# Optimization experiments

Hardware: AMD Instinct MI355X
Metric: run time of the kernel (lower is better)

The kernel has to match this reference:

```python
import math
import jax, jax.numpy as jnp
import numpy as np
from jax import lax

B, S, D = 2, 1024, 768
H, E, DH = 12, 8, 64          # n_head, num_experts, head dim
KA = 1                        # top-k experts per head (attention)
KF = 2                        # top-k experts per token (FFN)
DFF = 2048
EMA_DECAY = 0.99
CAP_FACTOR = 1.25
NEG_INF = -1e9


def setup_inputs() -> dict:
    key = jax.random.key(0)
    ks = jax.random.split(key, 16)
    sc = 0.02
    x = jax.random.normal(ks[0], (B, S, D), jnp.float32)
    causal = jnp.tril(jnp.ones((S, S), jnp.float32))
    mask = jnp.where(causal > 0, 0.0, NEG_INF).astype(jnp.float32)
    return {
        "x": x,
        "mask": mask,
        "W_q": jax.random.normal(ks[1], (D, D), jnp.float32) * sc,
        "W_k": jax.random.normal(ks[2], (D, D), jnp.float32) * sc,
        "W_v": jax.random.normal(ks[3], (H, E, DH, DH), jnp.float32) * sc,
        "W_o": jax.random.normal(ks[4], (H, E, DH, DH), jnp.float32) * sc,
        "W_router": jax.random.normal(ks[5], (D, H * E), jnp.float32) * sc,
        "g1": jnp.ones((D,), jnp.float32),
        "b1": jnp.zeros((D,), jnp.float32),
        "g2": jnp.ones((D,), jnp.float32),
        "b2": jnp.zeros((D,), jnp.float32),
        "gate_ff": jax.random.normal(ks[6], (D, E), jnp.float32) * sc,
        "W1": jax.random.normal(ks[7], (E, D, DFF), jnp.float32) * sc,
        "W2": jax.random.normal(ks[8], (E, DFF, D), jnp.float32) * sc,
    }


def layer_norm(x, g, b, eps=1e-5):
    m = jnp.mean(x, -1, keepdims=True)
    v = jnp.var(x, -1, keepdims=True)
    return (x - m) * lax.rsqrt(v + eps) * g + b


def head_switch_attention(x, mask, W_q, W_k, W_v, W_o, W_router):
    b, s, d = x.shape
    q = (x @ W_q).reshape(b, s, H, DH)
    k = (x @ W_k).reshape(b, s, H, DH)
    scores = jnp.einsum("bshd,bthd->bhst", q, k) / math.sqrt(DH) + mask
    p_attn = jax.nn.softmax(scores, axis=-1)          # (B,H,S,S)
    gate_logits = (x @ W_router).reshape(b, s, H, E)
    topk_scores, topk_idx = lax.top_k(gate_logits, KA)  # (B,S,H,KA)
    probs = jax.nn.softmax(topk_scores, axis=-1)
    x_h = x.reshape(b, s, H, DH)
    # value projections for all experts (small d_h x d_h GEMMs)
    v_all = jnp.einsum("bshd,hedf->bshef", x_h, W_v)
    y = jnp.zeros_like(x_h)
    hard_counts = jnp.zeros((H, E), jnp.float32)
    for slot in range(KA):
        oh = jax.nn.one_hot(topk_idx[..., slot], E, dtype=x.dtype)  # (B,S,H,E)
        v_sel = jnp.einsum("bshef,bshe->bshf", v_all, oh)
        # faithful to original einsum 'bhst,hbsd->hbtd' (sums over s)
        attn_out = jnp.einsum("bhst,bshf->bthf", p_attn, v_sel)
        o_all = jnp.einsum("bthf,hefg->btheg", attn_out, W_o)
        o_sel = jnp.einsum("btheg,bthe->bthg", o_all, oh)
        y = y + o_sel * probs[..., slot][..., None]
        hard_counts = hard_counts + lax.stop_gradient(oh).sum((0, 1))
    y = y.reshape(b, s, d)
    # EMA buffers start at zero -> ema = (1-decay)*hard/denom
    ema = hard_counts / (b * s * KA) * (1.0 - EMA_DECAY)
    p_lb = ema / (ema.sum() + 1e-9)
    aux = (p_lb * p_lb).sum() * E * H
    return y, aux


def moe_ffn(x, gate_ff, W1, W2):
    b, s, d = x.shape
    gate_logits = x @ gate_ff                      # (B,S,E), eval: no noise
    topk_scores, topk_idx = lax.top_k(gate_logits, KF)
    probs = jax.nn.softmax(topk_scores, axis=-1)   # (B,S,KF)
    capacity = math.ceil(CAP_FACTOR * (b * s) / E)
    flat_idx = topk_idx.reshape(-1)                # (B*S*KF,)
    oh_flat = jax.nn.one_hot(flat_idx, E, dtype=jnp.float32)
    tokens_so_far = jnp.cumsum(oh_flat, axis=0)
    keep = jnp.take_along_axis(tokens_so_far <= capacity, flat_idx[:, None], axis=1)[:, 0]
    probs = probs * keep.reshape(b, s, KF).astype(probs.dtype)
    probs = probs / (probs.sum(-1, keepdims=True) + 1e-9)
    oh = jax.nn.one_hot(topk_idx, E, dtype=probs.dtype)   # (B,S,KF,E)
    w = (probs[..., None] * oh).sum(2).reshape(b * s, E)  # combined weight per (token, expert)
    xf = x.reshape(b * s, d)
    yf = jnp.zeros_like(xf)
    for e in range(E):
        # scaling applied BEFORE ReLU, matching original x_sel = x * weight
        xe = xf * w[:, e:e + 1]
        yf = yf + jnp.maximum(xe @ W1[e], 0.0) @ W2[e]
    token_ctr = ((probs > 0)[..., None].astype(jnp.float32) * oh).sum((0, 1, 2))
    imp_ctr = (probs[..., None] * oh).sum((0, 1, 2))
    aux = ((token_ctr / token_ctr.sum()) * (imp_ctr / imp_ctr.sum())).sum() * E
    return yf.reshape(b, s, d), aux


def reference(x, mask, W_q, W_k, W_v, W_o, W_router, g1, b1, g2, b2, gate_ff, W1, W2):
    # pre-norm transformer block: x + Attn(LN(x)); x + MoEFFN(LN(x))
    a, aux1 = head_switch_attention(layer_norm(x, g1, b1), mask, W_q, W_k, W_v, W_o, W_router)
    x1 = x + a  # dropout is identity in eval
    f, aux2 = moe_ffn(layer_norm(x1, g2, b2), gate_ff, W1, W2)
    return x1 + f, aux1 + aux2
```

## Files before the change

### kernel.cpp

```cpp
#include <hip/hip_runtime.h>
#include <hip/hip_bf16.h>
#include <cstdint>

typedef __hip_bfloat16 bf16;
typedef __attribute__((ext_vector_type(8))) __bf16 bfrag;
typedef __attribute__((ext_vector_type(4))) float f32x4;

#define B_    2
#define S_    1024
#define D_    768
#define H_    12
#define E_    8
#define DH_   64
#define DFF_  2048
#define CAP_  320
#define CAPP_ 384
#define NTOK  (B_*S_)
#define NTH   (NTOK*H_)
#define QKLD  1536
#define NHE   (H_*E_)

__device__ __forceinline__ void stage16(const bf16* g, bf16* ldsLane){
#if __has_builtin(__builtin_amdgcn_global_load_lds)
  __builtin_amdgcn_global_load_lds((const __attribute__((address_space(1))) unsigned int*)g,
                                   (__attribute__((address_space(3))) unsigned int*)ldsLane, 16, 0, 0);
#else
  *(bfrag*)ldsLane = *(const bfrag*)g;
#endif
}

__device__ __forceinline__ void transp_tile_bf16(const float* __restrict__ src, bf16* __restrict__ dst,
                                                 int N, int K, int n0, int k0, int tid, float (*t)[64])
{
  int chunk = tid & 15, rgrp = tid >> 4;
#pragma unroll
  for (int rr=0; rr<8; rr++){
    int row = rr*16 + rgrp;
    float4 v = *(const float4*)(src + (long)(k0+row)*N + n0 + chunk*4);
    *(float4*)&t[row][((chunk ^ (row>>3)) & 15)*4] = v;
  }
  __syncthreads();
#pragma unroll
  for (int it=0; it<4; it++){
    int slot = it*256 + tid;
    int n = slot >> 4, kc = slot & 15;
    union { bfrag f; bf16 h[8]; } o;
#pragma unroll
    for (int i=0;i<8;i++){
      int row = kc*8 + i;
      o.h[i] = __float2bfloat16(t[row][n ^ (kc*4)]);
    }
    *(bfrag*)(dst + (long)(n0+n)*K + k0 + kc*8) = o.f;
  }
}

__global__ __launch_bounds__(256)
void transp_qkr(const float* __restrict__ Wq, const float* __restrict__ Wk,
                const float* __restrict__ Wr, bf16* __restrict__ WcatB, float* __restrict__ WrT)
{
  __shared__ float t[128][64];
  int bid = blockIdx.x, tid = threadIdx.x;
  if (bid < 144){
    const float* src; bf16* dst; int r;
    if (bid < 72){ src = Wq; dst = WcatB; r = bid; }
    else         { src = Wk; dst = WcatB + (long)768*768; r = bid - 72; }
    transp_tile_bf16(src, dst, 768, 768, (r%12)*64, (r/12)*128, tid, t);
  } else {
    int r = bid - 144;
    int n0 = (r % 3)*32, k0 = (r / 3)*64;
    int chunk = tid & 7, row2 = tid >> 3;
#pragma unroll
    for (int rr=0; rr<2; rr++){
      int row = rr*32 + row2;
      float4 v = *(const float4*)(Wr + (long)(k0+row)*96 + n0 + chunk*4);
      *(float4*)&t[row][chunk*4] = v;
    }
    __syncthreads();
    int chunkw = tid & 15, ng = tid >> 4;
#pragma unroll
    for (int rr=0; rr<2; rr++){
      int n = rr*16 + ng;
      float4 o;
      o.x = t[chunkw*4+0][n]; o.y = t[chunkw*4+1][n];
      o.z = t[chunkw*4+2][n]; o.w = t[chunkw*4+3][n];
      *(float4*)(WrT + (long)(n0+n)*768 + k0 + chunkw*4) = o;
    }
  }
}

__global__ __launch_bounds__(256)
void gemm_bn64(const bf16* __restrict__ A, const bf16* __restrict__ Bt,
               void* __restrict__ C, void* __restrict__ C2,
               int M, int N, int K, long sA, long sB, long sC, int relu, int outBf, int kSplit)
{
  int nwg = gridDim.x*gridDim.y*gridDim.z;
  int bid = blockIdx.x + gridDim.x*(blockIdx.y + gridDim.y*blockIdx.z);
  int nid = (bid & 7)*(nwg >> 3) + (bid >> 3);
  int bx = nid % gridDim.x;
  int t1 = nid / gridDim.x;
  int by = t1 % gridDim.y;
  int bz = t1 / gridDim.y;
  int e  = bz / kSplit, kc = bz - e*kSplit;
  A  += (long)e*sA;
  Bt += (long)e*sB;
  int kLen = K / kSplit, kBase = kc*kLen;
  int m0 = by*128, n0 = bx*64;
  __shared__ bf16 As[2][128*32];
  __shared__ bf16 Bs[2][64*32];
  int tid = threadIdx.x;
  int w = tid >> 6, lane = tid & 63;
  int quad = lane >> 4, l16 = lane & 15;
  int wm = w*32;
  f32x4 acc[2][4] = {};
  int srow = (lane >> 2);
  int gsw  = ((lane & 3) ^ (srow & 3))*8;
  const bf16* aBase = A + (long)m0*K;
  const bf16* bBase = Bt + (long)n0*K;
  int xr = (l16 & 3);
  int nIt = kLen >> 5;
  {
    int k0 = kBase;
#pragma unroll
    for (int j=0;j<2;j++){
      int c = w*2 + j, row = c*16 + srow;
      stage16(aBase + (long)row*K + k0 + gsw, As[0] + c*512 + lane*8);
    }
    int rowb = w*16 + srow;
    stage16(bBase + (long)rowb*K + k0 + gsw, Bs[0] + w*512 + lane*8);
  }
  int cur = 0;
  for (int it=0; it<nIt; ++it){
    __syncthreads();
    if (it+1 < nIt){
      int k0 = kBase + (it+1)*32;
      int nb = cur^1;
#pragma unroll
      for (int j=0;j<2;j++){
        int c = w*2 + j, row = c*16 + srow;
        stage16(aBase + (long)row*K + k0 + gsw, As[nb] + c*512 + lane*8);
      }
      int rowb = w*16 + srow;
      stage16(bBase + (long)rowb*K + k0 + gsw, Bs[nb] + w*512 + lane*8);
    }
    const bf16* Ac = As[cur];
    const bf16* Bc = Bs[cur];
    bfrag af[2], bfv[4];
#pragma unroll
    for (int t=0;t<2;t++) af[t]  = *(const bfrag*)(Ac + (wm + t*16 + l16)*32 + ((quad ^ xr)*8));
#pragma unroll
    for (int t=0;t<4;t++) bfv[t] = *(const bfrag*)(Bc + (t*16 + l16)*32 + ((quad ^ xr)*8));
#pragma unroll
    for (int ti=0;ti<2;ti++)
#pragma unroll
      for (int tj=0;tj<4;tj++)
        acc[ti][tj] = __builtin_amdgcn_mfma_f32_16x16x32_bf16(af[ti], bfv[tj], acc[ti][tj], 0, 0, 0);
    cur ^= 1;
  }
  long zoff = (long)e*sC;
  void* Cp = kc ? C2 : C;
  if (outBf){
    bf16* Cb = (bf16*)Cp + zoff;
#pragma unroll
    for (int ti=0;ti<2;ti++)
#pragma unroll
      for (int tj=0;tj<4;tj++)
#pragma unroll
        for (int r=0;r<4;r++){
          int row = m0 + wm + ti*16 + quad*4 + r;
          int col = n0 + tj*16 + l16;
          float v = acc[ti][tj][r];
          if (relu) v = fmaxf(v, 0.f);
          Cb[(long)row*N + col] = __float2bfloat16(v);
        }
  } else {
    float* Cf = (float*)Cp + zoff;
#pragma unroll
    for (int ti=0;ti<2;ti++)
#pragma unroll
      for (int tj=0;tj<4;tj++)
#pragma unroll
        for (int r=0;r<4;r++){
          int row = m0 + wm + ti*16 + quad*4 + r;
          int col = n0 + tj*16 + l16;
          float v = acc[ti][tj][r];
          if (relu) v = fmaxf(v, 0.f);
          Cf[(long)row*N + col] = v;
        }
  }
}

__global__ __launch_bounds__(256)
void gemm_ffn1(const float* __restrict__ ln2, const bf16* __restrict__ Bt, bf16* __restrict__ C,
               const int* __restrict__ lTok, const float* __restrict__ lW, const int* __restrict__ gCnt)
{
  int nwg = gridDim.x*gridDim.y*gridDim.z;
  int bid = blockIdx.x + gridDim.x*(blockIdx.y + gridDim.y*blockIdx.z);
  int nid = (bid & 7)*(nwg >> 3) + (bid >> 3);
  int bx = nid % gridDim.x;
  int t1 = nid / gridDim.x;
  int by = t1 % gridDim.y;
  int e  = t1 / gridDim.y;
  int m0 = by*128;
  const bf16* bBase = Bt + (long)e*2048*768 + (long)(bx*64)*768;
  __shared__ bf16 As[2][128*32];
  __shared__ bf16 Bs[2][64*32];
  int tid = threadIdx.x;
  int w = tid >> 6, lane = tid & 63;
  int quad = lane >> 4, l16 = lane & 15;
  int wm = w*32;
  f32x4 acc[2][4] = {};
  int srow = (lane >> 2);
  int gsw  = ((lane & 3) ^ (srow & 3))*8;
  int xr = (l16 & 3);
  int cnt = gCnt[e];
  int tokA[2]; float wA[2];
#pragma unroll
  for (int j=0;j<2;j++){
    int row = m0 + (w*2+j)*16 + srow;
    bool live = row < cnt;
    tokA[j] = live ? lTok[e*CAP_ + row] : 0;
    wA[j]   = live ? lW[e*CAP_ + row]   : 0.f;
  }
  const int nIt = 24;
  {
#pragma unroll
    for (int j=0;j<2;j++){
      const float* src = ln2 + (long)tokA[j]*D_ + gsw;
      float4 a0 = *(const float4*)(src);
      float4 a1 = *(const float4*)(src+4);
      union { bfrag f; bf16 h[8]; } o;
      o.h[0]=__float2bfloat16(a0.x*wA[j]); o.h[1]=__float2bfloat16(a0.y*wA[j]);
      o.h[2]=__float2bfloat16(a0.z*wA[j]); o.h[3]=__float2bfloat16(a0.w*wA[j]);
      o.h[4]=__float2bfloat16(a1.x*wA[j]); o.h[5]=__float2bfloat16(a1.y*wA[j]);
      o.h[6]=__float2bfloat16(a1.z*wA[j]); o.h[7]=__float2bfloat16(a1.w*wA[j]);
      *(bfrag*)(As[0] + (w*2+j)*512 + lane*8) = o.f;
    }
    int rowb = w*16 + srow;
    stage16(bBase + (long)rowb*768 + gsw, Bs[0] + w*512 + lane*8);
  }
  int cur = 0;
  for (int it=0; it<nIt; ++it){
    __syncthreads();
    float4 a0[2], a1[2];
    if (it+1 < nIt){
      int k0 = (it+1)*32;
#pragma unroll
      for (int j=0;j<2;j++){
        const float* src = ln2 + (long)tokA[j]*D_ + k0 + gsw;
        a0[j] = *(const float4*)(src);
        a1[j] = *(const float4*)(src+4);
      }
      int rowb = w*16 + srow;
      stage16(bBase + (long)rowb*768 + k0 + gsw, Bs[cur^1] + w*512 + lane*8);
    }
    const bf16* Ac = As[cur];
    const bf16* Bc = Bs[cur];
    bfrag af[2], bfv[4];
#pragma unroll
    for (int t=0;t<2;t++) af[t]  = *(const bfrag*)(Ac + (wm + t*16 + l16)*32 + ((quad ^ xr)*8));
#pragma unroll
    for (int t=0;t<4;t++) bfv[t] = *(const bfrag*)(Bc + (t*16 + l16)*32 + ((quad ^ xr)*8));
#pragma unroll
    for (int ti=0;ti<2;ti++)
#pragma unroll
      for (int tj=0;tj<4;tj++)
        acc[ti][tj] = __builtin_amdgcn_mfma_f32_16x16x32_bf16(af[ti], bfv[tj], acc[ti][tj], 0, 0, 0);
    if (it+1 < nIt){
      int nb = cur^1;
#pragma unroll
      for (int j=0;j<2;j++){
        union { bfrag f; bf16 h[8]; } o;
        o.h[0]=__float2bfloat16(a0[j].x*wA[j]); o.h[1]=__float2bfloat16(a0[j].y*wA[j]);
        o.h[2]=__float2bfloat16(a0[j].z*wA[j]); o.h[3]=__float2bfloat16(a0[j].w*wA[j]);
        o.h[4]=__float2bfloat16(a1[j].x*wA[j]); o.h[5]=__float2bfloat16(a1[j].y*wA[j]);
        o.h[6]=__float2bfloat16(a1[j].z*wA[j]); o.h[7]=__float2bfloat16(a1[j].w*wA[j]);
        *(bfrag*)(As[nb] + (w*2+j)*512 + lane*8) = o.f;
      }
    }
    cur ^= 1;
  }
  bf16* Cb = C + (long)e*CAPP_*DFF_;
#pragma unroll
  for (int ti=0;ti<2;ti++)
#pragma unroll
    for (int tj=0;tj<4;tj++)
#pragma unroll
      for (int r=0;r<4;r++){
        int row = m0 + wm + ti*16 + quad*4 + r;
        int col = bx*64 + tj*16 + l16;
        Cb[(long)row*DFF_ + col] = __float2bfloat16(fmaxf(acc[ti][tj][r], 0.f));
      }
}

__global__ __launch_bounds__(256)
void ln_kernel(const float* __restrict__ src, const float* __restrict__ g, const float* __restrict__ bb,
               float* __restrict__ dstF, bf16* __restrict__ dstB,
               const float* __restrict__ gateW, float* __restrict__ glog2)
{
  int row = blockIdx.x, tid = threadIdx.x;
  __shared__ float red[256];
  __shared__ float gsum[4][E_];
  float v[3];
#pragma unroll
  for (int j=0;j<3;j++) v[j] = src[(long)row*D_ + tid + j*256];
  float s = v[0]+v[1]+v[2];
  red[tid]=s; __syncthreads();
  for (int o=128;o>0;o>>=1){ if(tid<o) red[tid]+=red[tid+o]; __syncthreads(); }
  float mean = red[0]*(1.0f/D_);
  __syncthreads();
  float sq = 0.f;
#pragma unroll
  for (int j=0;j<3;j++){ float d=v[j]-mean; sq += d*d; }
  red[tid]=sq; __syncthreads();
  for (int o=128;o>0;o>>=1){ if(tid<o) red[tid]+=red[tid+o]; __syncthreads(); }
  float rstd = rsqrtf(red[0]*(1.0f/D_) + 1e-5f);
  float ov[3];
#pragma unroll
  for (int j=0;j<3;j++){
    int d = tid + j*256;
    float o = (v[j]-mean)*rstd*g[d] + bb[d];
    ov[j] = o;
    dstF[(long)row*D_+d] = o;
    if (dstB) dstB[(long)row*D_+d] = __float2bfloat16(o);
  }
  if (gateW){
    float gp[E_] = {};
#pragma unroll
    for (int j=0;j<3;j++){
      int d = tid + j*256;
      const float* gw = gateW + (long)d*E_;
#pragma unroll
      for (int e=0;e<E_;e++) gp[e] += ov[j]*gw[e];
    }
#pragma unroll
    for (int off=1; off<64; off<<=1)
#pragma unroll
      for (int e=0;e<E_;e++) gp[e] += __shfl_xor(gp[e], off);
    if ((tid & 63) == 0)
#pragma unroll
      for (int e=0;e<E_;e++) gsum[tid>>6][e] = gp[e];
    __syncthreads();
    if (tid < E_)
      glog2[(long)row*E_ + tid] = gsum[0][tid]+gsum[1][tid]+gsum[2][tid]+gsum[3][tid];
  }
}

#define RTOK 4
__global__ __launch_bounds__(768)
void router_argmax(const float* __restrict__ ln1, const float* __restrict__ WrT,
                   int* __restrict__ eidx, int* __restrict__ gHist,
                   int* __restrict__ hCnt, int* __restrict__ hList)
{
  int tok0 = blockIdx.x*RTOK;
  int tid = threadIdx.x;
  int col = tid >> 3, seg = tid & 7;
  __shared__ float xrow[RTOK][D_];
  __shared__ float logits[RTOK][96];
  for (int i=tid; i<RTOK*D_; i+=768){
    int t = i / D_, dpos = i - t*D_;
    xrow[t][dpos] = ln1[(long)(tok0+t)*D_ + dpos];
  }
  __syncthreads();
  const float* wrow = WrT + (long)col*D_;
  float acc[RTOK] = {};
#pragma unroll
  for (int j=0;j<24;j++){
    int dbase = j*32 + seg*4;
    float4 w = *(const float4*)(wrow + dbase);
#pragma unroll
    for (int t=0;t<RTOK;t++){
      float4 xv = *(const float4*)(&xrow[t][dbase]);
      acc[t] += xv.x*w.x + xv.y*w.y + xv.z*w.z + xv.w*w.w;
    }
  }
#pragma unroll
  for (int off=1; off<8; off<<=1)
#pragma unroll
    for (int t=0;t<RTOK;t++) acc[t] += __shfl_xor(acc[t], off);
  if (seg == 0)
#pragma unroll
    for (int t=0;t<RTOK;t++) logits[t][col] = acc[t];
  __syncthreads();
  if (tid < RTOK*H_){
    int t = tid / H_, h = tid % H_;
    const float* p = &logits[t][h*8];
    float best = p[0]; int bi = 0;
#pragma unroll
    for (int e=1;e<8;e++){ float v=p[e]; if (v > best){ best=v; bi=e; } }
    int tok = tok0 + t;
    eidx[tok*H_ + h] = bi;
    atomicAdd(&gHist[h*E_ + bi], 1);
    int he = h*E_ + bi;
    int pos = atomicAdd(&hCnt[he], 1);
    hList[he*NTOK + pos] = tok;
  }
}

__global__ __launch_bounds__(256)
void vsel_b(const float* __restrict__ ln1, const float* __restrict__ Wv,
            const int* __restrict__ hCnt, const int* __restrict__ hList,
            bf16* __restrict__ vT)
{
  int he = blockIdx.x;
  int h = he >> 3;
  __shared__ float Ws[DH_*DH_];
  __shared__ float xsh[4][DH_];
  int tid = threadIdx.x;
  const float* W = Wv + (long)he*DH_*DH_;
  for (int i=tid; i<DH_*DH_; i+=256) Ws[i] = W[i];
  int cnt = hCnt[he];
  __syncthreads();
  int w = tid >> 6, lane = tid & 63;
  const int* lst = hList + (long)he*NTOK;
  for (int i = blockIdx.y*4 + w; i < cnt; i += 32){
    int tok = lst[i];
    int b = tok >> 10, s = tok & 1023;
    xsh[w][lane] = ln1[(long)tok*D_ + h*DH_ + lane];
    float acc = 0.f;
#pragma unroll 8
    for (int d=0; d<DH_; d++) acc += xsh[w][d]*Ws[d*DH_ + lane];
    vT[((long)(b*H_+h)*DH_ + lane)*S_ + s] = __float2bfloat16(acc);
  }
}

__global__ __launch_bounds__(256)
void attn_stats_mfma(const bf16* __restrict__ qkB, float* __restrict__ gM, float* __restrict__ gL,
                     const float* __restrict__ W1, const float* __restrict__ W2,
                     bf16* __restrict__ WT1, bf16* __restrict__ WT2)
{
  __shared__ __align__(16) char smem[32768];
  int tid = threadIdx.x;
  if (blockIdx.z >= 2){
    int flat = (blockIdx.z - 2)*96 + blockIdx.y*8 + blockIdx.x;
    const float* src; int N, K, bx, by; bf16* dst;
    if (flat < 1536){ int e = flat/192, r = flat - e*192;
      src = W1 + (long)e*768*2048; N = 2048; K = 768;  bx = r % 32; by = r / 32;
      dst = WT1 + (long)e*2048*768;
    } else { int f2 = flat - 1536; int e = f2/192, r = f2 - e*192;
      src = W2 + (long)e*2048*768; N = 768;  K = 2048; bx = r % 12; by = r / 12;
      dst = WT2 + (long)e*768*2048;
    }
    transp_tile_bf16(src, dst, N, K, bx*64, by*128, tid, (float(*)[64])smem);
    return;
  }
  bf16* ldsQ = (bf16*)smem;
  int h = blockIdx.y, b = blockIdx.z;
  int w = tid >> 6, lane = tid & 63;
  int quad = lane >> 4, l16 = lane & 15;
  int x7 = l16 & 7;
  const bf16* kbase = qkB + ((long)(b*S_))*QKLD + 768 + h*DH_;
  for (int half=0; half<2; half++){
    int s0 = (half ? (S_/64 - 1 - blockIdx.x) : blockIdx.x)*64;
    __syncthreads();
    const bf16* qbase = qkB + ((long)(b*S_ + s0))*QKLD + h*DH_;
#pragma unroll
    for (int j=0;j<2;j++){
      int c = j*256 + tid;
      int row = c >> 3;
      int gs = ((c & 7) ^ (row & 7))*8;
      stage16(qbase + (long)row*QKLD + gs, ldsQ + c*8);
      stage16(kbase + (long)row*QKLD + gs, (bf16*)(smem + 8192) + c*8);
    }
    float m_ln[4] = {-1e30f,-1e30f,-1e30f,-1e30f};
    float l_ln[4] = {0.f,0.f,0.f,0.f};
    int ttEnd = s0 >> 6;
    int cur = 0;
    for (int tt=0; tt<=ttEnd; tt++){
      __syncthreads();
      if (tt < ttEnd){
        bf16* Kn = (bf16*)(smem + 8192 + ((cur^1) << 13));
#pragma unroll
        for (int j=0;j<2;j++){
          int c = j*256 + tid;
          int row = c >> 3;
          int gs = ((c & 7) ^ (row & 7))*8;
          stage16(kbase + (long)((tt+1)*64 + row)*QKLD + gs, Kn + c*8);
        }
      }
      const bf16* Kc = (const bf16*)(smem + 8192 + (cur << 13));
      bfrag af0 = *(const bfrag*)(ldsQ + (w*16 + l16)*64 + ((quad     ^ x7)*8));
      bfrag af1 = *(const bfrag*)(ldsQ + (w*16 + l16)*64 + (((quad+4) ^ x7)*8));
      f32x4 cfr[4];
#pragma unroll
      for (int j=0;j<4;j++){
        bfrag b0 = *(const bfrag*)(Kc + (j*16 + l16)*64 + ((quad     ^ x7)*8));
        bfrag b1 = *(const bfrag*)(Kc + (j*16 + l16)*64 + (((quad+4) ^ x7)*8));
        f32x4 z = {};
        z = __builtin_amdgcn_mfma_f32_16x16x32_bf16(af0, b0, z, 0,0,0);
        z = __builtin_amdgcn_mfma_f32_16x16x32_bf16(af1, b1, z, 0,0,0);
        cfr[j] = z;
      }
#pragma unroll
      for (int r=0;r<4;r++){
        int s_g = s0 + w*16 + quad*4 + r;
        float v0 = (tt*64      + l16 <= s_g) ? cfr[0][r]*0.125f : -1e30f;
        float v1 = (tt*64 + 16 + l16 <= s_g) ? cfr[1][r]*0.125f : -1e30f;
        float v2 = (tt*64 + 32 + l16 <= s_g) ? cfr[2][r]*0.125f : -1e30f;
        float v3 = (tt*64 + 48 + l16 <= s_g) ? cfr[3][r]*0.125f : -1e30f;
        float mt = fmaxf(fmaxf(v0,v1), fmaxf(v2,v3));
        float mn = fmaxf(m_ln[r], mt);
        l_ln[r] = l_ln[r]*__expf(m_ln[r]-mn)
                + ((__expf(v0-mn)+__expf(v1-mn)) + (__expf(v2-mn)+__expf(v3-mn)));
        m_ln[r] = mn;
      }
      cur ^= 1;
    }
#pragma unroll
    for (int r=0;r<4;r++){
      float mf = m_ln[r];
#pragma unroll
      for (int mm=1; mm<16; mm<<=1) mf = fmaxf(mf, __shfl_xor(mf, mm));
      float lf = l_ln[r]*__expf(m_ln[r]-mf);
#pragma unroll
      for (int mm=1; mm<16; mm<<=1) lf += __shfl_xor(lf, mm);
      if (l16 == 0){
        long basei = ((long)(b*H_ + h))*S_ + s0 + w*16 + quad*4 + r;
        gM[basei] = mf; gL[basei] = lf;
      }
    }
  }
}

__global__ __launch_bounds__(256)
void attn_pv(const bf16* __restrict__ qkB, const bf16* __restrict__ vT,
             const float* __restrict__ gM, const float* __restrict__ gL, float* __restrict__ aoH)
{
  int h = blockIdx.y, b = blockIdx.z;
  int bh = b*H_ + h;
  int tid = threadIdx.x;
  int w = tid >> 6, lane = tid & 63;
  int quad = lane >> 4, l16 = lane & 15;
  int x7 = l16 & 7;
  __shared__ bf16 ldsK[64*64];
  __shared__ bf16 ldsQ[2][64*64];
  __shared__ bf16 ldsV[2][64*64];
  __shared__ bf16 ldsS[64*72];
  __shared__ float smx[2][64], sli[2][64];
  const bf16* qbase = qkB + ((long)(b*S_))*QKLD + h*DH_;
  const bf16* vbase = vT + ((long)bh*DH_)*S_;
  for (int half=0; half<2; half++){
    int t0 = (half ? (S_/64 - 1 - blockIdx.x) : blockIdx.x)*64;
    __syncthreads();
    const bf16* kbase = qkB + ((long)(b*S_ + t0))*QKLD + 768 + h*DH_;
    int sb0 = t0 >> 6;
#pragma unroll
    for (int j=0;j<2;j++){
      int c = j*256 + tid;
      int row = c >> 3;
      int gs = ((c & 7) ^ (row & 7))*8;
      stage16(kbase + (long)row*QKLD + gs, ldsK + c*8);
      stage16(qbase + (long)(sb0*64 + row)*QKLD + gs, ldsQ[0] + c*8);
      stage16(vbase + (long)row*S_ + sb0*64 + gs, ldsV[0] + c*8);
    }
    if (tid < 64){
      smx[0][tid] = gM[(long)bh*S_ + sb0*64 + tid];
      sli[0][tid] = 1.0f / gL[(long)bh*S_ + sb0*64 + tid];
    }
    f32x4 accO[4] = {};
    int cur = 0;
    for (int sb = sb0; sb < S_/64; sb++){
      __syncthreads();
      if (sb+1 < S_/64){
        int nb = cur^1;
#pragma unroll
        for (int j=0;j<2;j++){
          int c = j*256 + tid;
          int row = c >> 3;
          int gs = ((c & 7) ^ (row & 7))*8;
          stage16(qbase + (long)((sb+1)*64 + row)*QKLD + gs, ldsQ[nb] + c*8);
          stage16(vbase + (long)row*S_ + (sb+1)*64 + gs, ldsV[nb] + c*8);
        }
        if (tid < 64){
          smx[nb][tid] = gM[(long)bh*S_ + (sb+1)*64 + tid];
          sli[nb][tid] = 1.0f / gL[(long)bh*S_ + (sb+1)*64 + tid];
        }
      }
      const bf16* Qc = ldsQ[cur];
      const bf16* Vc = ldsV[cur];
      bfrag af0 = *(const bfrag*)(ldsK + (w*16 + l16)*64 + ((quad     ^ x7)*8));
      bfrag af1 = *(const bfrag*)(ldsK + (w*16 + l16)*64 + (((quad+4) ^ x7)*8));
      f32x4 cs[4];
#pragma unroll
      for (int j=0;j<4;j++){
        bfrag b0 = *(const bfrag*)(Qc + (j*16 + l16)*64 + ((quad     ^ x7)*8));
        bfrag b1 = *(const bfrag*)(Qc + (j*16 + l16)*64 + (((quad+4) ^ x7)*8));
        f32x4 z = {};
        z = __builtin_amdgcn_mfma_f32_16x16x32_bf16(af0, b0, z, 0,0,0);
        z = __builtin_amdgcn_mfma_f32_16x16x32_bf16(af1, b1, z, 0,0,0);
        cs[j] = z;
      }
#pragma unroll
      for (int j=0;j<4;j++)
#pragma unroll
        for (int r=0;r<4;r++){
          int t_loc = w*16 + quad*4 + r;
          int s_loc = j*16 + l16;
          float wgt = ((t0 + t_loc) <= (sb*64 + s_loc))
                    ? __expf(cs[j][r]*0.125f - smx[cur][s_loc])*sli[cur][s_loc] : 0.f;
          ldsS[t_loc*72 + s_loc] = __float2bfloat16(wgt);
        }
      bfrag pa0 = *(const bfrag*)(ldsS + (w*16 + l16)*72 + quad*8);
      bfrag pa1 = *(const bfrag*)(ldsS + (w*16 + l16)*72 + 32 + quad*8);
#pragma unroll
      for (int j=0;j<4;j++){
        bfrag b0 = *(const bfrag*)(Vc + (j*16 + l16)*64 + ((quad     ^ x7)*8));
        bfrag b1 = *(const bfrag*)(Vc + (j*16 + l16)*64 + (((quad+4) ^ x7)*8));
        accO[j] = __builtin_amdgcn_mfma_f32_16x16x32_bf16(pa0, b0, accO[j], 0,0,0);
        accO[j] = __builtin_amdgcn_mfma_f32_16x16x32_bf16(pa1, b1, accO[j], 0,0,0);
      }
      cur ^= 1;
    }
#pragma unroll
    for (int j=0;j<4;j++)
#pragma unroll
      for (int r=0;r<4;r++){
        int t_loc = w*16 + quad*4 + r;
        int f = j*16 + l16;
        aoH[((long)bh*S_ + t0 + t_loc)*DH_ + f] = accO[j][r];
      }
  }
}

__global__ __launch_bounds__(256)
void oproj_b(const float* __restrict__ aoH, const float* __restrict__ Wo,
             const int* __restrict__ hCnt, const int* __restrict__ hList,
             const float* __restrict__ x, float* __restrict__ x1)
{
  int he = blockIdx.x;
  int h = he >> 3;
  __shared__ float Ws[DH_*DH_];
  __shared__ float xsh[4][DH_];
  int tid = threadIdx.x;
  const float* W = Wo + (long)he*DH_*DH_;
  for (int i=tid; i<DH_*DH_; i+=256) Ws[i] = W[i];
  int cnt = hCnt[he];
  __syncthreads();
  int w = tid >> 6, lane = tid & 63;
  const int* lst = hList + (long)he*NTOK;
  for (int i = blockIdx.y*4 + w; i < cnt; i += 32){
    int tok = lst[i];
    int b = tok >> 10, s = tok & 1023;
    xsh[w][lane] = aoH[((long)(b*H_+h)*S_ + s)*DH_ + lane];
    float acc = 0.f;
#pragma unroll 8
    for (int f=0; f<DH_; f++) acc += xsh[w][f]*Ws[f*DH_ + lane];
    long idx = (long)tok*D_ + h*DH_ + lane;
    x1[idx] = x[idx] + acc;
  }
}

__global__ __launch_bounds__(256)
void route_kernel(const float* __restrict__ glog2, const int* __restrict__ gHist,
                  int* __restrict__ gI0, int* __restrict__ gI1,
                  int* __restrict__ gPos0, int* __restrict__ gPos1,
                  int* __restrict__ listTok, float* __restrict__ listW,
                  int* __restrict__ gCnt, float* __restrict__ auxOut)
{
  __shared__ unsigned char sI0[NTOK], sI1[NTOK];
  __shared__ float sP0[NTOK], sP1[NTOK];
  __shared__ short sPos0[NTOK], sPos1[NTOK];
  __shared__ int   sScan[256*E_];
  __shared__ int   sHist[H_*E_];
  __shared__ float sImp[E_];
  __shared__ int   sCnt[E_];
  int tid = threadIdx.x;
  if (tid < E_) sImp[tid] = 0.f;
  if (tid < H_*E_) sHist[tid] = gHist[tid];
  for (int i=tid; i<NTOK; i+=256){
    const float* p = glog2 + (long)i*E_;
    float b0 = p[0]; int e0 = 0;
#pragma unroll
    for (int e=1;e<E_;e++){ float vv=p[e]; if (vv > b0){ b0=vv; e0=e; } }
    float b1v = -1e30f; int e1 = 0;
#pragma unroll
    for (int e=0;e<E_;e++){ if (e==e0) continue; float vv=p[e]; if (vv > b1v){ b1v=vv; e1=e; } }
    float ex = __expf(b1v - b0);
    float inv = 1.f/(1.f + ex);
    sI0[i] = (unsigned char)e0; sI1[i] = (unsigned char)e1;
    sP0[i] = inv; sP1[i] = ex*inv;
    gI0[i] = e0; gI1[i] = e1;
  }
  __syncthreads();
  {
    int myCnt[E_] = {};
#pragma unroll
    for (int j=0;j<16;j++){
      int i = tid*16 + j;
      int tok = i >> 1;
      int e = (i & 1) ? (int)sI1[tok] : (int)sI0[tok];
      myCnt[e]++;
    }
#pragma unroll
    for (int e=0;e<E_;e++) sScan[tid*E_+e] = myCnt[e];
    __syncthreads();
    for (int off=1; off<256; off<<=1){
      int v[E_];
      if (tid >= off){
#pragma unroll
        for (int e=0;e<E_;e++) v[e] = sScan[(tid-off)*E_+e];
      }
      __syncthreads();
      if (tid >= off){
#pragma unroll
        for (int e=0;e<E_;e++) sScan[tid*E_+e] += v[e];
      }
      __syncthreads();
    }
    int pref[E_];
#pragma unroll
    for (int e=0;e<E_;e++) pref[e] = tid ? sScan[(tid-1)*E_+e] : 0;
#pragma unroll
    for (int j=0;j<16;j++){
      int i = tid*16 + j;
      int tok = i >> 1;
      int e = (i & 1) ? (int)sI1[tok] : (int)sI0[tok];
      int pos = pref[e]++;
      short p = (pos < CAP_) ? (short)pos : (short)-1;
      if (i & 1) sPos1[tok] = p; else sPos0[tok] = p;
    }
    if (tid < E_){
      int cnt = sScan[255*E_ + tid];
      sCnt[tid] = cnt < CAP_ ? cnt : CAP_;
      gCnt[tid] = sCnt[tid];
    }
  }
  __syncthreads();
  for (int i=tid; i<NTOK; i+=256){
    int e0 = sI0[i], e1 = sI1[i];
    int p0i = sPos0[i], p1i = sPos1[i];
    float k0 = p0i >= 0 ? 1.f : 0.f, k1 = p1i >= 0 ? 1.f : 0.f;
    float p0 = sP0[i], p1 = sP1[i];
    float denom = p0*k0 + p1*k1 + 1e-9f;
    float w0 = p0*k0/denom, w1 = p1*k1/denom;
    if (p0i >= 0){ listTok[e0*CAP_+p0i] = i; listW[e0*CAP_+p0i] = w0; atomicAdd(&sImp[e0], w0); }
    if (p1i >= 0){ listTok[e1*CAP_+p1i] = i; listW[e1*CAP_+p1i] = w1; atomicAdd(&sImp[e1], w1); }
    gPos0[i] = p0i; gPos1[i] = p1i;
  }
  __syncthreads();
  if (tid == 0){
    float tot = 0.f;
    for (int i=0;i<H_*E_;i++) tot += (float)sHist[i]*(1.0f/NTOK)*0.01f;
    float a1 = 0.f;
    for (int i=0;i<H_*E_;i++){
      float p = ((float)sHist[i]*(1.0f/NTOK)*0.01f)/(tot + 1e-9f);
      a1 += p*p;
    }
    a1 *= (float)(H_*E_);
    float tcs = 0.f, ims = 0.f;
    for (int e=0;e<E_;e++){ tcs += (float)sCnt[e]; ims += sImp[e]; }
    float a2 = 0.f;
    for (int e=0;e<E_;e++) a2 += ((float)sCnt[e]/tcs)*(sImp[e]/ims);
    a2 *= (float)E_;
    auxOut[0] = a1 + a2;
  }
}

__global__ __launch_bounds__(256)
void combine_kernel(const float* __restrict__ x1,
                    const float* __restrict__ Ya, const float* __restrict__ Yb,
                    const int* __restrict__ gI0, const int* __restrict__ gI1,
                    const int* __restrict__ gPos0, const int* __restrict__ gPos1,
                    float* __restrict__ out)
{
  int i = blockIdx.x;
  int tid = threadIdx.x;
  int p0 = gPos0[i], p1 = gPos1[i];
  int e0 = gI0[i],  e1 = gI1[i];
  long off0 = (long)(e0*CAPP_ + (p0 >= 0 ? p0 : 0))*D_;
  long off1 = (long)(e1*CAPP_ + (p1 >= 0 ? p1 : 0))*D_;
  const float* y0a = Ya + off0; const float* y0b = Yb + off0;
  const float* y1a = Ya + off1; const float* y1b = Yb + off1;
  for (int d=tid; d<D_; d+=256){
    float v = x1[(long)i*D_+d];
    if (p0 >= 0) v += y0a[d] + y0b[d];
    if (p1 >= 0) v += y1a[d] + y1b[d];
    out[(long)i*D_+d] = v;
  }
}

extern "C" void kernel_launch(void* const* d_in, const int* in_sizes, int n_in,
                              void* d_out, int out_size, void* d_ws, size_t ws_size,
                              hipStream_t stream)
{
  const float* x    = (const float*)d_in[0];
  const float* W_q  = (const float*)d_in[2];
  const float* W_k  = (const float*)d_in[3];
  const float* W_v  = (const float*)d_in[4];
  const float* W_o  = (const float*)d_in[5];
  const float* W_r  = (const float*)d_in[6];
  const float* g1   = (const float*)d_in[7];
  const float* b1   = (const float*)d_in[8];
  const float* g2   = (const float*)d_in[9];
  const float* b2   = (const float*)d_in[10];
  const float* gate = (const float*)d_in[11];
  const float* W1   = (const float*)d_in[12];
  const float* W2   = (const float*)d_in[13];
  float* out = (float*)d_out;

  float* wsf = (float*)d_ws;
  const long oX1   = 0;
  const long oLnF  = 1572864;
  const long oLnB  = 3145728;
  const long oWcat = 3932160;
  const long oWrT  = 4521984;
  const long oHist = 4595712;
  const long oHCnt = 4595808;
  const long oGM   = 4718592;
  const long oGL   = 4743168;
  const long oEidx = 4767744;
  const long oGlg2 = 4792320;
  const long oI0   = 4808704;
  const long oI1   = 4810752;
  const long oP0   = 4812800;
  const long oP1   = 4814848;
  const long oLT   = 4816896;
  const long oLW   = 4819456;
  const long oCnt  = 4822016;
  const long SB    = 4822528;
  const long oWT1  = SB + 12976128;
  const long oWT2  = oWT1 + 6291456;
  const long TOTAL = oWT2 + 6291456;
  if (ws_size < (size_t)TOTAL*4) return;

  float* x1    = wsf + oX1;
  float* lnbF  = wsf + oLnF;
  bf16*  lnbB  = (bf16*)(wsf + oLnB);
  bf16*  WcatB = (bf16*)(wsf + oWcat);
  float* WrT   = wsf + oWrT;
  int*   gHist = (int*)(wsf + oHist);
  int*   hCnt  = (int*)(wsf + oHCnt);
  float* gM    = wsf + oGM;
  float* gL    = wsf + oGL;
  int*   eidx  = (int*)(wsf + oEidx);
  float* glog2 = wsf + oGlg2;
  int*   gI0   = (int*)(wsf + oI0);
  int*   gI1   = (int*)(wsf + oI1);
  int*   gPos0 = (int*)(wsf + oP0);
  int*   gPos1 = (int*)(wsf + oP1);
  int*   lTok  = (int*)(wsf + oLT);
  float* lW    = wsf + oLW;
  int*   gCnt  = (int*)(wsf + oCnt);
  bf16*  qkB   = (bf16*)(wsf + SB);
  bf16*  vT    = (bf16*)(wsf + SB + 1572864);
  float* aoH   = wsf + SB + 2359296;
  int*   hList = (int*)(wsf + SB + 3932160);
  bf16*  Hid   = (bf16*)(wsf + SB + 7471104);
  float* Yexp  = wsf + SB + 10616832;
  float* YexpB = wsf + oLnF;
  bf16*  WT1   = (bf16*)(wsf + oWT1);
  bf16*  WT2   = (bf16*)(wsf + oWT2);

  (void)hipMemsetAsync(gHist, 0, 2*NHE*sizeof(int), stream);
  transp_qkr<<<180,256,0,stream>>>(W_q, W_k, W_r, WcatB, WrT);

  ln_kernel<<<NTOK,256,0,stream>>>(x, g1, b1, lnbF, lnbB, nullptr, nullptr);
  gemm_bn64<<<dim3(24,16,1),256,0,stream>>>(lnbB, WcatB, qkB, nullptr, 2048, QKLD, 768, 0,0,0, 0, 1, 1);
  router_argmax<<<NTOK/RTOK,768,0,stream>>>(lnbF, WrT, eidx, gHist, hCnt, hList);
  vsel_b<<<dim3(NHE,8,1),256,0,stream>>>(lnbF, W_v, hCnt, hList, vT);
  attn_stats_mfma<<<dim3(S_/128,H_,2+32),256,0,stream>>>(qkB, gM, gL, W1, W2, WT1, WT2);
  attn_pv<<<dim3(S_/128,H_,B_),256,0,stream>>>(qkB, vT, gM, gL, aoH);
  oproj_b<<<dim3(NHE,8,1),256,0,stream>>>(aoH, W_o, hCnt, hList, x, x1);

  ln_kernel<<<NTOK,256,0,stream>>>(x1, g2, b2, lnbF, nullptr, gate, glog2);
  route_kernel<<<1,256,0,stream>>>(glog2, gHist, gI0,gI1,gPos0,gPos1, lTok,lW,gCnt, out + (size_t)NTOK*D_);
  gemm_ffn1<<<dim3(32,3,8),256,0,stream>>>(lnbF, WT1, Hid, lTok, lW, gCnt);
  gemm_bn64<<<dim3(12,3,16),256,0,stream>>>(Hid, WT2, Yexp, YexpB, CAPP_, 768, 2048,
                                            (long)CAPP_*2048, (long)768*2048, (long)CAPP_*768, 0, 0, 2);
  combine_kernel<<<NTOK,256,0,stream>>>(x1, Yexp, YexpB, gI0,gI1,gPos0,gPos1, out);
}
```

Baseline: 382.2 us.

## Rewrite single-block routing with 1024 threads and wave-shuffle scans

The single-block route kernel now runs 1024 threads instead of 256. The per-expert prefix scan, which used a shared-memory Hillis-Steele scan with many __syncthreads, becomes a wavefront __shfl_up scan plus a small cross-wave combine. The importance sums move from shared-memory atomics to per-thread accumulators reduced with shuffles. The aim is to cut barrier and serialization latency in this serial single-block stage, at the cost of more register pressure per thread.

Measured after the change: 381.4 us. About the same (-0.2%).

```diff
diff --git a/kernel.cpp b/kernel.cpp
--- a/kernel.cpp
+++ b/kernel.cpp
@@ -649,7 +649,7 @@
   }
 }
 
-__global__ __launch_bounds__(256)
+__global__ __launch_bounds__(1024)
 void route_kernel(const float* __restrict__ glog2, const int* __restrict__ gHist,
                   int* __restrict__ gI0, int* __restrict__ gI1,
                   int* __restrict__ gPos0, int* __restrict__ gPos1,
@@ -659,14 +659,15 @@
   __shared__ unsigned char sI0[NTOK], sI1[NTOK];
   __shared__ float sP0[NTOK], sP1[NTOK];
   __shared__ short sPos0[NTOK], sPos1[NTOK];
-  __shared__ int   sScan[256*E_];
-  __shared__ int   sHist[H_*E_];
+  __shared__ int   waveTot[16][E_];
+  __shared__ float waveImp[16][E_];
   __shared__ float sImp[E_];
+  __shared__ int   sHist[NHE];
   __shared__ int   sCnt[E_];
   int tid = threadIdx.x;
-  if (tid < E_) sImp[tid] = 0.f;
-  if (tid < H_*E_) sHist[tid] = gHist[tid];
-  for (int i=tid; i<NTOK; i+=256){
+  int lane = tid & 63, wv = tid >> 6;
+  if (tid < NHE) sHist[tid] = gHist[tid];
+  for (int i=tid; i<NTOK; i+=1024){
     const float* p = glog2 + (long)i*E_;
     float b0 = p[0]; int e0 = 0;
 #pragma unroll
@@ -681,67 +682,98 @@
     gI0[i] = e0; gI1[i] = e1;
   }
   __syncthreads();
-  {
-    int myCnt[E_] = {};
-#pragma unroll
-    for (int j=0;j<16;j++){
-      int i = tid*16 + j;
-      int tok = i >> 1;
-      int e = (i & 1) ? (int)sI1[tok] : (int)sI0[tok];
-      myCnt[e]++;
-    }
-#pragma unroll
-    for (int e=0;e<E_;e++) sScan[tid*E_+e] = myCnt[e];
-    __syncthreads();
-    for (int off=1; off<256; off<<=1){
-      int v[E_];
-      if (tid >= off){
-#pragma unroll
-        for (int e=0;e<E_;e++) v[e] = sScan[(tid-off)*E_+e];
-      }
-      __syncthreads();
-      if (tid >= off){
-#pragma unroll
-        for (int e=0;e<E_;e++) sScan[tid*E_+e] += v[e];
-      }
-      __syncthreads();
-    }
-    int pref[E_];
-#pragma unroll
-    for (int e=0;e<E_;e++) pref[e] = tid ? sScan[(tid-1)*E_+e] : 0;
-#pragma unroll
-    for (int j=0;j<16;j++){
-      int i = tid*16 + j;
-      int tok = i >> 1;
-      int e = (i & 1) ? (int)sI1[tok] : (int)sI0[tok];
-      int pos = pref[e]++;
-      short p = (pos < CAP_) ? (short)pos : (short)-1;
-      if (i & 1) sPos1[tok] = p; else sPos0[tok] = p;
-    }
-    if (tid < E_){
-      int cnt = sScan[255*E_ + tid];
-      sCnt[tid] = cnt < CAP_ ? cnt : CAP_;
-      gCnt[tid] = sCnt[tid];
-    }
-  }
-  __syncthreads();
-  for (int i=tid; i<NTOK; i+=256){
+  int myCnt[E_] = {};
+  unsigned char ie[4];
+  int base = tid*4;
+#pragma unroll
+  for (int j=0;j<4;j++){
+    int i = base + j;
+    int tok = i >> 1;
+    int e = (i & 1) ? (int)sI1[tok] : (int)sI0[tok];
+    ie[j] = (unsigned char)e;
+#pragma unroll
+    for (int ee=0;ee<E_;ee++) myCnt[ee] += (e == ee);
+  }
+  int inc[E_];
+#pragma unroll
+  for (int e=0;e<E_;e++) inc[e] = myCnt[e];
+#pragma unroll
+  for (int off=1; off<64; off<<=1){
+#pragma unroll
+    for (int e=0;e<E_;e++){
+      int v = __shfl_up(inc[e], off);
+      if (lane >= off) inc[e] += v;
+    }
+  }
+  if (lane == 63)
+#pragma unroll
+    for (int e=0;e<E_;e++) waveTot[wv][e] = inc[e];
+  __syncthreads();
+  int pref[E_];
+#pragma unroll
+  for (int e=0;e<E_;e++) pref[e] = inc[e] - myCnt[e];
+  for (int w2=0; w2<16; w2++){
+    if (w2 < wv){
+#pragma unroll
+      for (int e=0;e<E_;e++) pref[e] += waveTot[w2][e];
+    }
+  }
+#pragma unroll
+  for (int j=0;j<4;j++){
+    int i = base + j;
+    int tok = i >> 1;
+    int pos = 0;
+#pragma unroll
+    for (int ee=0;ee<E_;ee++) if (ie[j] == ee) pos = pref[ee]++;
+    short p = (pos < CAP_) ? (short)pos : (short)-1;
+    if (i & 1) sPos1[tok] = p; else sPos0[tok] = p;
+  }
+  if (tid < E_){
+    int cnt = 0;
+    for (int w2=0; w2<16; w2++) cnt += waveTot[w2][tid];
+    sCnt[tid] = cnt < CAP_ ? cnt : CAP_;
+    gCnt[tid] = sCnt[tid];
+  }
+  __syncthreads();
+  float impLoc[E_] = {};
+  for (int i=tid; i<NTOK; i+=1024){
     int e0 = sI0[i], e1 = sI1[i];
     int p0i = sPos0[i], p1i = sPos1[i];
     float k0 = p0i >= 0 ? 1.f : 0.f, k1 = p1i >= 0 ? 1.f : 0.f;
     float p0 = sP0[i], p1 = sP1[i];
     float denom = p0*k0 + p1*k1 + 1e-9f;
     float w0 = p0*k0/denom, w1 = p1*k1/denom;
-    if (p0i >= 0){ listTok[e0*CAP_+p0i] = i; listW[e0*CAP_+p0i] = w0; atomicAdd(&sImp[e0], w0); }
-    if (p1i >= 0){ listTok[e1*CAP_+p1i] = i; listW[e1*CAP_+p1i] = w1; atomicAdd(&sImp[e1], w1); }
+    if (p0i >= 0){
+      listTok[e0*CAP_+p0i] = i; listW[e0*CAP_+p0i] = w0;
+#pragma unroll
+      for (int ee=0;ee<E_;ee++) impLoc[ee] += (e0 == ee) ? w0 : 0.f;
+    }
+    if (p1i >= 0){
+      listTok[e1*CAP_+p1i] = i; listW[e1*CAP_+p1i] = w1;
+#pragma unroll
+      for (int ee=0;ee<E_;ee++) impLoc[ee] += (e1 == ee) ? w1 : 0.f;
+    }
     gPos0[i] = p0i; gPos1[i] = p1i;
+  }
+#pragma unroll
+  for (int off=1; off<64; off<<=1)
+#pragma unroll
+    for (int e=0;e<E_;e++) impLoc[e] += __shfl_xor(impLoc[e], off);
+  if (lane == 0)
+#pragma unroll
+    for (int e=0;e<E_;e++) waveImp[wv][e] = impLoc[e];
+  __syncthreads();
+  if (tid < E_){
+    float s = 0.f;
+    for (int w2=0; w2<16; w2++) s += waveImp[w2][tid];
+    sImp[tid] = s;
   }
   __syncthreads();
   if (tid == 0){
     float tot = 0.f;
-    for (int i=0;i<H_*E_;i++) tot += (float)sHist[i]*(1.0f/NTOK)*0.01f;
+    for (int i=0;i<NHE;i++) tot += (float)sHist[i]*(1.0f/NTOK)*0.01f;
     float a1 = 0.f;
-    for (int i=0;i<H_*E_;i++){
+    for (int i=0;i<NHE;i++){
       float p = ((float)sHist[i]*(1.0f/NTOK)*0.01f)/(tot + 1e-9f);
       a1 += p*p;
     }
@@ -862,7 +894,7 @@
   oproj_b<<<dim3(NHE,8,1),256,0,stream>>>(aoH, W_o, hCnt, hList, x, x1);
 
   ln_kernel<<<NTOK,256,0,stream>>>(x1, g2, b2, lnbF, nullptr, gate, glog2);
-  route_kernel<<<1,256,0,stream>>>(glog2, gHist, gI0,gI1,gPos0,gPos1, lTok,lW,gCnt, out + (size_t)NTOK*D_);
+  route_kernel<<<1,1024,0,stream>>>(glog2, gHist, gI0,gI1,gPos0,gPos1, lTok,lW,gCnt, out + (size_t)NTOK*D_);
   gemm_ffn1<<<dim3(32,3,8),256,0,stream>>>(lnbF, WT1, Hid, lTok, lW, gCnt);
   gemm_bn64<<<dim3(12,3,16),256,0,stream>>>(Hid, WT2, Yexp, YexpB, CAPP_, 768, 2048,
                                             (long)CAPP_*2048, (long)768*2048, (long)CAPP_*768, 0, 0, 2);
```
